# Kernel tuning notes

Measured on AMD Instinct MI355X. Metric: run time of the kernel, lower is better.

Reference implementation:

```python
import jax, jax.numpy as jnp
import numpy as np

B, LQ, LKV, E, H, D, P = 2, 2048, 2048, 1024, 16, 64, 64
NEG = -1e10


def setup_inputs() -> dict:
    key = jax.random.key(0)
    ks = jax.random.split(key, 8)
    inputs_q = jax.random.normal(ks[0], (B, LQ, E), jnp.float32)
    inputs_kv = jax.random.normal(ks[1], (B, LKV, E), jnp.float32)
    key_prefix = jax.random.normal(ks[2], (B, P, H, D), jnp.float32)
    value_prefix = jax.random.normal(ks[3], (B, P, H, D), jnp.float32)
    # causal mask, broadcastable over heads: [B, 1, LQ, LKV]
    mask = jnp.broadcast_to(jnp.tril(jnp.ones((LQ, LKV), bool)), (B, 1, LQ, LKV))
    scale = 1.0 / np.sqrt(E)  # fan_in variance scaling
    Wq = jax.random.normal(ks[4], (E, H, D), jnp.float32) * scale
    Wk = jax.random.normal(ks[5], (E, H, D), jnp.float32) * scale
    Wv = jax.random.normal(ks[6], (E, H, D), jnp.float32) * scale
    Wo = jax.random.normal(ks[7], (H, D, E), jnp.float32) * (1.0 / np.sqrt(H * D))
    return dict(inputs_q=inputs_q, inputs_kv=inputs_kv, key_prefix=key_prefix,
                value_prefix=value_prefix, mask=mask, Wq=Wq, Wk=Wk, Wv=Wv, Wo=Wo)


def reference(inputs_q, inputs_kv, key_prefix, value_prefix, mask, Wq, Wk, Wv, Wo):
    depth_scaling = jnp.sqrt(jnp.asarray(D, inputs_q.dtype))
    # query kernel is divided by sqrt(head_dim) at init -> fold into projection
    q = jnp.einsum('bqe,ehd->bqhd', inputs_q, Wq) / depth_scaling
    k = jnp.einsum('bke,ehd->bkhd', inputs_kv, Wk)
    v = jnp.einsum('bke,ehd->bkhd', inputs_kv, Wv)
    # prefix concat on the key/value length axis
    k = jnp.concatenate([key_prefix, k], axis=1)   # [B, P+LKV, H, D]
    v = jnp.concatenate([value_prefix, v], axis=1)
    # mask -> additive bias; prefix tokens get zero bias (always attendable)
    bias = jnp.where(mask, 0.0, NEG).astype(inputs_q.dtype)      # [B,1,LQ,LKV]
    prefix_bias = jnp.zeros(bias.shape[:-1] + (P,), bias.dtype)  # [B,1,LQ,P]
    bias = jnp.concatenate([prefix_bias, bias], axis=-1)         # [B,1,LQ,P+LKV]
    scores = jnp.einsum('bqhd,bkhd->bhqk', q, k) + bias
    probs = jax.nn.softmax(scores, axis=-1)
    ctx = jnp.einsum('bhqk,bkhd->bqhd', probs, v)
    return jnp.einsum('bqhd,hde->bqe', ctx, Wo)
```

## Files before the change

### kernel.cpp

```cpp
#include <hip/hip_runtime.h>
#include <hip/hip_bf16.h>

#define B_   2
#define LQ_  2048
#define LKV_ 2048
#define E_   1024
#define H_   16
#define D_   64
#define P_   64
#define LT_  (P_ + LKV_)
#define NEG_ -1e10f
#define LOG2E_ 1.4426950408889634f

typedef unsigned short ushort_t;
typedef unsigned int   uint_t;
typedef float f32x4   __attribute__((ext_vector_type(4)));
typedef float f32x16  __attribute__((ext_vector_type(16)));
typedef short bf16x8  __attribute__((ext_vector_type(8)));
typedef uint_t u32x4  __attribute__((ext_vector_type(4)));

__device__ __forceinline__ ushort_t f2bf(float f) {
    union { float f; uint_t u; } v; v.f = f;
    return (ushort_t)((v.u + 0x7fffu + ((v.u >> 16) & 1u)) >> 16);
}

__device__ __forceinline__ uint_t cvt_pk_bf16(float lo, float hi) {
    uint_t r;
    asm("v_cvt_pk_bf16_f32 %0, %1, %2" : "=v"(r) : "v"(lo), "v"(hi));
    return r;
}

__device__ __forceinline__ float exp2x(float x) {
    float r;
    asm("v_exp_f32 %0, %1" : "=v"(r) : "v"(x));
    return r;
}

__device__ __forceinline__ float bflo(uint_t u) {
    return __builtin_bit_cast(float, u << 16);
}
__device__ __forceinline__ float bfhi(uint_t u) {
    return __builtin_bit_cast(float, u & 0xFFFF0000u);
}


#define GLOAD16(gp, lp)                                                     \
    __builtin_amdgcn_global_load_lds(                                       \
        (const __attribute__((address_space(1))) void*)(gp),                \
        (__attribute__((address_space(3))) void*)(lp), 16, 0, 0)

__global__ __launch_bounds__(256) void prep(
    const float* __restrict__ iq, const float* __restrict__ ikv,
    const float* __restrict__ w0, const float* __restrict__ w1,
    const float* __restrict__ w2, const float* __restrict__ w3,
    const float* __restrict__ kp, const float* __restrict__ vp,
    ushort_t* __restrict__ Aq, ushort_t* __restrict__ Akv,
    ushort_t* __restrict__ d0, ushort_t* __restrict__ d1,
    ushort_t* __restrict__ d2, ushort_t* __restrict__ d3,
    ushort_t* __restrict__ kws, ushort_t* __restrict__ vws)
{
    __shared__ float t[32][33];
    const int blk = blockIdx.x;
    const int tid = threadIdx.x;

    if (blk < 8192) {
        const int idx = blk * 256 + tid;
        constexpr int HALF = 4096 * 1024 / 4;
        const float4 v = (idx < HALF) ? ((const float4*)iq)[idx]
                                      : ((const float4*)ikv)[idx - HALF];
        const uint2 p = make_uint2((uint_t)f2bf(v.x) | ((uint_t)f2bf(v.y) << 16),
                                   (uint_t)f2bf(v.z) | ((uint_t)f2bf(v.w) << 16));
        if (idx < HALF) ((uint2*)Aq)[idx] = p;
        else            ((uint2*)Akv)[idx - HALF] = p;
    } else if (blk < 12288) {
        const int tr = blk - 8192;
        const int bz = tr >> 10, rem = tr & 1023;
        const int x0 = (rem & 31) * 32, y0 = (rem >> 5) * 32;
        const float* S = (bz == 0) ? w0 : (bz == 1) ? w1 : (bz == 2) ? w2 : w3;
        ushort_t* D = (bz == 0) ? d0 : (bz == 1) ? d1 : (bz == 2) ? d2 : d3;
        const int tx = tid & 31, ty = tid >> 5;
        #pragma unroll
        for (int i = 0; i < 4; ++i)
            t[ty + i * 8][tx] = S[(size_t)(y0 + ty + i * 8) * 1024 + x0 + tx];
        __syncthreads();
        #pragma unroll
        for (int i = 0; i < 4; ++i)
            D[(size_t)(x0 + ty + i * 8) * 1024 + (y0 + tx)] =
                f2bf(t[tx][ty + i * 8]);
    } else {
        const int idx = (blk - 12288) * 256 + tid;
        const int d4 = idx & 15;
        const int h  = (idx >> 4) & 15;
        const int p  = (idx >> 8) & 63;
        const int b  = idx >> 14;
        const float4 kv = ((const float4*)kp)[idx];
        const float4 vv = ((const float4*)vp)[idx];
        const size_t kdst = ((size_t)(b * H_ + h) * LT_ + p) * D_ + d4 * 4;
        *(uint2*)(kws + kdst) =
            make_uint2((uint_t)f2bf(kv.x) | ((uint_t)f2bf(kv.y) << 16),
                       (uint_t)f2bf(kv.z) | ((uint_t)f2bf(kv.w) << 16));
        const float* vs = (const float*)&vv;
        #pragma unroll
        for (int i = 0; i < 4; ++i)
            vws[((size_t)(b * H_ + h) * D_ + d4 * 4 + i) * LT_ + p] = f2bf(vs[i]);
    }
}

__device__ __forceinline__ void gemm_core(const ushort_t* __restrict__ A,
                                          const ushort_t* __restrict__ Wt,
                                          ushort_t* As, ushort_t* Bs,
                                          int m0, int n0, f32x4 (*acc)[4])
{
    constexpr int K = 1024, NSTEP = 16;
    const int tid  = threadIdx.x;
    const int lane = tid & 63;
    const int wave = tid >> 6;
    const int l15 = lane & 15, lg = lane >> 4;
    const int wr = (wave >> 1) * 32;
    const int wc = (wave & 1) * 64;
    const uint_t xr = (uint_t)((l15 & 7) << 4);

    for (int i = 0; i < NSTEP; ++i) {
        const int k0 = i * 64;
        #pragma unroll
        for (int j = 0; j < 2; ++j) {
            const int c = j * 256 + tid;
            const int row = c >> 3, cc = c & 7;
            const size_t so = (size_t)row * K + k0 + ((cc ^ (row & 7)) * 8);
            GLOAD16(A + (size_t)m0 * K + so, (char*)As + (j * 256 + wave * 64) * 16);
        }
        #pragma unroll
        for (int j = 0; j < 4; ++j) {
            const int c = j * 256 + tid;
            const int row = c >> 3, cc = c & 7;
            const size_t so = (size_t)row * K + k0 + ((cc ^ (row & 7)) * 8);
            GLOAD16(Wt + (size_t)n0 * K + so, (char*)Bs + (j * 256 + wave * 64) * 16);
        }
        asm volatile("s_waitcnt vmcnt(0)" ::: "memory");
        __builtin_amdgcn_s_barrier();

        bf16x8 af[2][2], bfr[2][4];
        #pragma unroll
        for (int kt = 0; kt < 2; ++kt) {
            #pragma unroll
            for (int mt = 0; mt < 2; ++mt)
                af[kt][mt] = *(const bf16x8*)((const char*)As + (wr + mt * 16 + l15) * 128
                                              + ((kt * 64 + lg * 16) ^ xr));
            #pragma unroll
            for (int nt = 0; nt < 4; ++nt)
                bfr[kt][nt] = *(const bf16x8*)((const char*)Bs + (wc + nt * 16 + l15) * 128
                                               + ((kt * 64 + lg * 16) ^ xr));
        }
        #pragma unroll
        for (int mt = 0; mt < 2; ++mt)
            #pragma unroll
            for (int nt = 0; nt < 4; ++nt) {
                acc[mt][nt] = __builtin_amdgcn_mfma_f32_16x16x32_bf16(
                    af[0][mt], bfr[0][nt], acc[mt][nt], 0, 0, 0);
                acc[mt][nt] = __builtin_amdgcn_mfma_f32_16x16x32_bf16(
                    af[1][mt], bfr[1][nt], acc[mt][nt], 0, 0, 0);
            }

        __builtin_amdgcn_s_barrier();
    }
}

__global__ __launch_bounds__(256) void gemm_qkv(
    const ushort_t* __restrict__ Aq, const ushort_t* __restrict__ Akv,
    const ushort_t* __restrict__ WqT, const ushort_t* __restrict__ WkT,
    const ushort_t* __restrict__ WvT,
    ushort_t* __restrict__ qws, ushort_t* __restrict__ kws,
    ushort_t* __restrict__ vws)
{
    __shared__ __align__(16) ushort_t As[64 * 64];
    __shared__ __align__(16) ushort_t Bs[128 * 64];
    const int by = blockIdx.y, sel = by >> 3;
    const ushort_t* A  = sel ? Akv : Aq;
    const ushort_t* Wt = (sel == 0) ? WqT : (sel == 1) ? WkT : WvT;
    const float scale  = sel ? 1.0f : 0.125f * LOG2E_;
    const int m0 = blockIdx.x * 64, n0 = (by & 7) * 128;

    f32x4 acc[2][4];
    #pragma unroll
    for (int mt = 0; mt < 2; ++mt)
        #pragma unroll
        for (int nt = 0; nt < 4; ++nt) acc[mt][nt] = (f32x4)0.f;

    gemm_core(A, Wt, As, Bs, m0, n0, acc);

    const int lane = threadIdx.x & 63, wave = threadIdx.x >> 6;
    const int l15 = lane & 15, lg = lane >> 4;
    const int wr = (wave >> 1) * 32, wc = (wave & 1) * 64;

    if (sel == 2) {
        #pragma unroll
        for (int mt = 0; mt < 2; ++mt)
            #pragma unroll
            for (int nt = 0; nt < 4; ++nt) {
                const int n = n0 + wc + nt * 16 + l15;
                const int h = n >> 6, d = n & 63;
                const int m = m0 + wr + mt * 16 + lg * 4;
                const int bb = m >> 11, ll = m & 2047;
                const uint2 pk = make_uint2(
                    (uint_t)f2bf(acc[mt][nt][0]) | ((uint_t)f2bf(acc[mt][nt][1]) << 16),
                    (uint_t)f2bf(acc[mt][nt][2]) | ((uint_t)f2bf(acc[mt][nt][3]) << 16));
                *(uint2*)(vws + ((size_t)(bb * H_ + h) * D_ + d) * LT_ + P_ + ll) = pk;
            }
    } else {
        ushort_t* Cw     = (sel == 0) ? qws : kws;
        const int Lout   = (sel == 0) ? LQ_ : LT_;
        const int rowoff = (sel == 0) ? 0 : P_;
        #pragma unroll
        for (int mt = 0; mt < 2; ++mt)
            #pragma unroll
            for (int nt = 0; nt < 4; ++nt) {
                const int n = n0 + wc + nt * 16 + l15;
                const int h = n >> 6, d = n & 63;
                #pragma unroll
                for (int r = 0; r < 4; ++r) {
                    const int m = m0 + wr + mt * 16 + lg * 4 + r;
                    const int bb = m >> 11, ll = m & 2047;
                    Cw[(((size_t)(bb * H_ + h) * Lout) + (rowoff + ll)) * D_ + d] =
                        f2bf(acc[mt][nt][r] * scale);
                }
            }
    }
}

__global__ __launch_bounds__(256) void gemm_out(const ushort_t* __restrict__ A,
                                                const ushort_t* __restrict__ Wt,
                                                float* __restrict__ C)
{
    __shared__ __align__(16) ushort_t As[64 * 64];
    __shared__ __align__(16) ushort_t Bs[128 * 64];
    const int m0 = blockIdx.x * 64, n0 = blockIdx.y * 128;

    f32x4 acc[2][4];
    #pragma unroll
    for (int mt = 0; mt < 2; ++mt)
        #pragma unroll
        for (int nt = 0; nt < 4; ++nt) acc[mt][nt] = (f32x4)0.f;

    gemm_core(A, Wt, As, Bs, m0, n0, acc);

    const int lane = threadIdx.x & 63, wave = threadIdx.x >> 6;
    const int l15 = lane & 15, lg = lane >> 4;
    const int wr = (wave >> 1) * 32, wc = (wave & 1) * 64;
    #pragma unroll
    for (int mt = 0; mt < 2; ++mt)
        #pragma unroll
        for (int nt = 0; nt < 4; ++nt) {
            const int n = n0 + wc + nt * 16 + l15;
            #pragma unroll
            for (int r = 0; r < 4; ++r) {
                const int m = m0 + wr + mt * 16 + lg * 4 + r;
                C[(size_t)m * 1024 + n] = acc[mt][nt][r];
            }
        }
}

__global__ __launch_bounds__(256) void attn_mfma(const ushort_t* __restrict__ qws,
                                                 const ushort_t* __restrict__ kws,
                                                 const ushort_t* __restrict__ vws,
                                                 ushort_t* __restrict__ pO,
                                                 float* __restrict__ ml)
{
    const int tid  = threadIdx.x;
    const int lane = tid & 63;
    const int wave = tid >> 6;
    const int z    = blockIdx.x;
    const int slot = z >> 8;
    const int c    = z & 255;
    const int g    = c >> 5;
    const int bh   = c & 31;
    const int seg  = slot >> 1;
    const int qb   = (slot & 1) ? g : (15 - g);

    const ushort_t* Qg  = qws + (size_t)bh * LQ_ * D_;
    const ushort_t* Kg  = kws + (size_t)bh * LT_ * D_;
    const ushort_t* Vtg = vws + (size_t)bh * D_ * LT_;

    __shared__ __align__(16) ushort_t Ks[2 * 64 * 64];
    __shared__ __align__(16) ushort_t Vt[2 * 64 * 64];

    const int l31 = lane & 31;
    const int hi  = lane >> 5;
    const uint_t xsw = (uint_t)((l31 & 7) << 4);
    const int qbase = qb * 128 + wave * 32;
    const int q     = qbase + l31;
    const int qe    = qbase + 31;

    bf16x8 qf[4];
    #pragma unroll
    for (int kd = 0; kd < 4; ++kd)
        qf[kd] = *(const bf16x8*)(Qg + (size_t)q * D_ + kd * 16 + hi * 8);

    f32x16 acc[2];
    acc[0] = (f32x16)0.f;
    acc[1] = (f32x16)0.f;
    float lpreg = 0.f;

    const int ntile = 2 * qb + 3;
    const int i0    = seg ? (qb + 2) : 0;
    const int iend  = seg ? ntile : (qb + 2);

    auto STAGE = [&](int t, int par) {
        const int t0s = t * 64;
        char* kd = (char*)Ks + par * 8192;
        char* vd = (char*)Vt + par * 8192;
        #pragma unroll
        for (int i = 0; i < 2; ++i) {
            const int c2 = i * 256 + tid;
            const int rr = c2 >> 3, cc = c2 & 7;
            GLOAD16(Kg + (size_t)(t0s + rr) * D_ + ((cc ^ (rr & 7)) * 8),
                    kd + (i * 256 + wave * 64) * 16);
            GLOAD16(Vtg + (size_t)rr * LT_ + t0s + ((cc ^ (rr & 7)) * 8),
                    vd + (i * 256 + wave * 64) * 16);
        }
    };

    STAGE(i0, 0);
    STAGE(i0 + 1, 1);

    for (int i = i0; i < iend; ++i) {
        const int t0 = i * 64;
        const int cur = (i - i0) & 1;
        if (i + 1 < iend) {
            asm volatile("s_waitcnt vmcnt(4)" ::: "memory");
        } else {
            asm volatile("s_waitcnt vmcnt(0)" ::: "memory");
        }
        __builtin_amdgcn_s_barrier();

        if (t0 <= P_ + qe) {
            const char* KsB = (const char*)Ks + cur * 8192;
            const char* VtB = (const char*)Vt + cur * 8192;

            f32x16 sv[2];
            __builtin_amdgcn_s_setprio(1);
            #pragma unroll
            for (int th = 0; th < 2; ++th) {
                f32x16 zf = (f32x16)0.f;
                #pragma unroll
                for (int kd = 0; kd < 4; ++kd) {
                    const bf16x8 a = *(const bf16x8*)(
                        KsB + (th * 32 + l31) * 128 + ((kd * 32 + hi * 16) ^ xsw));
                    zf = __builtin_amdgcn_mfma_f32_32x32x16_bf16(a, qf[kd], zf, 0, 0, 0);
                }
                sv[th] = zf;
            }
            __builtin_amdgcn_s_setprio(0);

            if (t0 + 63 > P_ + qbase) {
                #pragma unroll
                for (int th = 0; th < 2; ++th)
                    #pragma unroll
                    for (int r = 0; r < 16; ++r) {
                        const int t = t0 + th * 32 + (r & 3) + 8 * (r >> 2) + 4 * hi;
                        if (!(t < P_ || (t - P_) <= q)) sv[th][r] += NEG_;
                    }
            }

            #pragma unroll
            for (int th = 0; th < 2; ++th)
                #pragma unroll
                for (int r = 0; r < 16; ++r)
                    sv[th][r] = exp2x(sv[th][r]);
            {
                float t16[16];
                #pragma unroll
                for (int r = 0; r < 16; ++r) t16[r] = sv[0][r] + sv[1][r];
                float t8[8];
                #pragma unroll
                for (int r = 0; r < 8; ++r) t8[r] = t16[r] + t16[r + 8];
                float t4[4];
                #pragma unroll
                for (int r = 0; r < 4; ++r) t4[r] = t8[r] + t8[r + 4];
                lpreg += (t4[0] + t4[1]) + (t4[2] + t4[3]);
            }

            bf16x8 pb[4];
            #pragma unroll
            for (int kt = 0; kt < 4; ++kt) {
                const int th = kt >> 1, base = (kt & 1) * 8;
                uint4 w;
                w.x = cvt_pk_bf16(sv[th][base + 0], sv[th][base + 1]);
                w.y = cvt_pk_bf16(sv[th][base + 2], sv[th][base + 3]);
                w.z = cvt_pk_bf16(sv[th][base + 4], sv[th][base + 5]);
                w.w = cvt_pk_bf16(sv[th][base + 6], sv[th][base + 7]);
                pb[kt] = __builtin_bit_cast(bf16x8, w);
            }

            __builtin_amdgcn_s_setprio(1);
            #pragma unroll
            for (int dh = 0; dh < 2; ++dh) {
                const char* rowp = VtB + (dh * 32 + l31) * 128 + 8 * hi;
                #pragma unroll
                for (int kt = 0; kt < 4; ++kt) {
                    const uint_t off = ((uint_t)(kt * 32)) ^ xsw;
                    const uint2 va = *(const uint2*)(rowp + off);
                    const uint2 vb = *(const uint2*)(rowp + (off ^ 16));
                    uint4 w;
                    w.x = va.x; w.y = va.y; w.z = vb.x; w.w = vb.y;
                    const bf16x8 vfr = __builtin_bit_cast(bf16x8, w);
                    acc[dh] = __builtin_amdgcn_mfma_f32_32x32x16_bf16(
                        vfr, pb[kt], acc[dh], 0, 0, 0);
                }
            }
            __builtin_amdgcn_s_setprio(0);
        }

        __builtin_amdgcn_s_barrier();
        if (i + 2 < iend) STAGE(i + 2, cur);
    }

    const float ltot = lpreg + __shfl_xor(lpreg, 32);
    const size_t qrow = (size_t)(seg * 32 + bh) * 2048 + q;
    #pragma unroll
    for (int dh = 0; dh < 2; ++dh)
        #pragma unroll
        for (int gg = 0; gg < 4; ++gg) {
            const int d = dh * 32 + gg * 8 + hi * 4;
            const uint2 pk = make_uint2(
                cvt_pk_bf16(acc[dh][4 * gg + 0], acc[dh][4 * gg + 1]),
                cvt_pk_bf16(acc[dh][4 * gg + 2], acc[dh][4 * gg + 3]));
            *(uint2*)(pO + qrow * 64 + d) = pk;
        }
    if (hi == 0)
        ml[qrow] = ltot;
}

__global__ __launch_bounds__(256) void attn_merge(const ushort_t* __restrict__ pO,
                                                  const float* __restrict__ ml,
                                                  ushort_t* __restrict__ ctx)
{
    const int idx = blockIdx.x * 256 + threadIdx.x;
    const int dg = idx & 15;
    const int q  = (idx >> 4) & 2047;
    const int bh = idx >> 15;
    const int b = bh >> 4, h = bh & 15;

    const size_t q0 = (size_t)bh * 2048 + q;
    const size_t q1 = (size_t)(32 + bh) * 2048 + q;
    const float inv = 1.0f / (ml[q0] + ml[q1]);

    const uint2 a0 = *(const uint2*)(pO + q0 * 64 + dg * 4);
    const uint2 a1 = *(const uint2*)(pO + q1 * 64 + dg * 4);
    const float o0 = (bflo(a0.x) + bflo(a1.x)) * inv;
    const float o1 = (bfhi(a0.x) + bfhi(a1.x)) * inv;
    const float o2 = (bflo(a0.y) + bflo(a1.y)) * inv;
    const float o3 = (bfhi(a0.y) + bfhi(a1.y)) * inv;

    const uint2 pk = make_uint2(
        (uint_t)f2bf(o0) | ((uint_t)f2bf(o1) << 16),
        (uint_t)f2bf(o2) | ((uint_t)f2bf(o3) << 16));
    *(uint2*)(ctx + (((size_t)b * LQ_ + q) * H_ + h) * D_ + dg * 4) = pk;
}

extern "C" void kernel_launch(void* const* d_in, const int* in_sizes, int n_in,
                              void* d_out, int out_size, void* d_ws, size_t ws_size,
                              hipStream_t stream)
{
    const float* inputs_q     = (const float*)d_in[0];
    const float* inputs_kv    = (const float*)d_in[1];
    const float* key_prefix   = (const float*)d_in[2];
    const float* value_prefix = (const float*)d_in[3];
    const float* Wq = (const float*)d_in[5];
    const float* Wk = (const float*)d_in[6];
    const float* Wv = (const float*)d_in[7];
    const float* Wo = (const float*)d_in[8];
    float* out = (float*)d_out;

    ushort_t* Aq  = (ushort_t*)d_ws;
    ushort_t* Akv = Aq  + (size_t)4096 * 1024;
    ushort_t* WqT = Akv + (size_t)4096 * 1024;
    ushort_t* WkT = WqT + (size_t)1024 * 1024;
    ushort_t* WvT = WkT + (size_t)1024 * 1024;
    ushort_t* WoT = WvT + (size_t)1024 * 1024;
    ushort_t* qws = WoT + (size_t)1024 * 1024;
    ushort_t* kws = qws + (size_t)B_ * H_ * LQ_ * D_;
    ushort_t* vws = kws + (size_t)B_ * H_ * LT_ * D_;
    ushort_t* ctx = vws + (size_t)B_ * H_ * LT_ * D_;

    ushort_t* pO    = Aq;
    float*    mlbuf = (float*)WqT;

    prep<<<12416, 256, 0, stream>>>(inputs_q, inputs_kv, Wq, Wk, Wv, Wo,
                                    key_prefix, value_prefix,
                                    Aq, Akv, WqT, WkT, WvT, WoT, kws, vws);
    gemm_qkv<<<dim3(64, 24), 256, 0, stream>>>(Aq, Akv, WqT, WkT, WvT,
                                               qws, kws, vws);
    attn_mfma<<<2 * B_ * H_ * (LQ_ / 128), 256, 0, stream>>>(qws, kws, vws,
                                                             pO, mlbuf);
    attn_merge<<<4096, 256, 0, stream>>>(pO, mlbuf, ctx);
    gemm_out<<<dim3(64, 8), 256, 0, stream>>>(ctx, WoT, out);
}
```

Measured before the change: 118.1 us.

## Split long causal query blocks into three KV segments for better load balance

The attention kernel now splits the heavier query blocks (qb 8-15) across three KV-range segments instead of two, so each workgroup does a smaller, more even share of the causal work. The grid grows from 1024 to 1280 blocks. Partial outputs of the third segment go to an extra buffer, and the merge kernel adds them in for those rows. This reduces tail imbalance on the long blocks, at the cost of more partial-result traffic and more re-reads of Q.

```diff
diff --git a/kernel.cpp b/kernel.cpp
--- a/kernel.cpp
+++ b/kernel.cpp
@@ -263,18 +263,32 @@
                                                  const ushort_t* __restrict__ kws,
                                                  const ushort_t* __restrict__ vws,
                                                  ushort_t* __restrict__ pO,
+                                                 ushort_t* __restrict__ pO2,
                                                  float* __restrict__ ml)
 {
     const int tid  = threadIdx.x;
     const int lane = tid & 63;
     const int wave = tid >> 6;
     const int z    = blockIdx.x;
-    const int slot = z >> 8;
-    const int c    = z & 255;
-    const int g    = c >> 5;
-    const int bh   = c & 31;
-    const int seg  = slot >> 1;
-    const int qb   = (slot & 1) ? g : (15 - g);
+
+    int qb, bh, s, i0, iend;
+    if (z < 768) {
+        s  = z >> 8;
+        qb = 8 + ((z >> 5) & 7);
+        bh = z & 31;
+        const int nt = 2 * qb + 3;
+        const int n0 = (nt + 2) / 3, n1 = (nt + 1) / 3;
+        i0   = (s == 0) ? 0 : ((s == 1) ? n0 : n0 + n1);
+        iend = (s == 0) ? n0 : ((s == 1) ? n0 + n1 : nt);
+    } else {
+        const int y = z - 768;
+        s  = y >> 8;
+        qb = 7 - ((y >> 5) & 7);
+        bh = y & 31;
+        const int nt = 2 * qb + 3;
+        i0   = s ? (qb + 2) : 0;
+        iend = s ? nt : (qb + 2);
+    }
 
     const ushort_t* Qg  = qws + (size_t)bh * LQ_ * D_;
     const ushort_t* Kg  = kws + (size_t)bh * LT_ * D_;
@@ -299,10 +313,6 @@
     acc[0] = (f32x16)0.f;
     acc[1] = (f32x16)0.f;
     float lpreg = 0.f;
-
-    const int ntile = 2 * qb + 3;
-    const int i0    = seg ? (qb + 2) : 0;
-    const int iend  = seg ? ntile : (qb + 2);
 
     auto STAGE = [&](int t, int par) {
         const int t0s = t * 64;
@@ -415,22 +425,39 @@
     }
 
     const float ltot = lpreg + __shfl_xor(lpreg, 32);
-    const size_t qrow = (size_t)(seg * 32 + bh) * 2048 + q;
-    #pragma unroll
-    for (int dh = 0; dh < 2; ++dh)
-        #pragma unroll
-        for (int gg = 0; gg < 4; ++gg) {
-            const int d = dh * 32 + gg * 8 + hi * 4;
-            const uint2 pk = make_uint2(
-                cvt_pk_bf16(acc[dh][4 * gg + 0], acc[dh][4 * gg + 1]),
-                cvt_pk_bf16(acc[dh][4 * gg + 2], acc[dh][4 * gg + 3]));
-            *(uint2*)(pO + qrow * 64 + d) = pk;
-        }
-    if (hi == 0)
-        ml[qrow] = ltot;
+    if (z < 768 && s == 2) {
+        const size_t e2 = (size_t)((qb - 8) * 32 + bh) * 128 + (q & 127);
+        #pragma unroll
+        for (int dh = 0; dh < 2; ++dh)
+            #pragma unroll
+            for (int gg = 0; gg < 4; ++gg) {
+                const int d = dh * 32 + gg * 8 + hi * 4;
+                const uint2 pk = make_uint2(
+                    cvt_pk_bf16(acc[dh][4 * gg + 0], acc[dh][4 * gg + 1]),
+                    cvt_pk_bf16(acc[dh][4 * gg + 2], acc[dh][4 * gg + 3]));
+                *(uint2*)(pO2 + e2 * 64 + d) = pk;
+            }
+        if (hi == 0)
+            ml[2 * 32 * 2048 + e2] = ltot;
+    } else {
+        const size_t qrow = (size_t)(s * 32 + bh) * 2048 + q;
+        #pragma unroll
+        for (int dh = 0; dh < 2; ++dh)
+            #pragma unroll
+            for (int gg = 0; gg < 4; ++gg) {
+                const int d = dh * 32 + gg * 8 + hi * 4;
+                const uint2 pk = make_uint2(
+                    cvt_pk_bf16(acc[dh][4 * gg + 0], acc[dh][4 * gg + 1]),
+                    cvt_pk_bf16(acc[dh][4 * gg + 2], acc[dh][4 * gg + 3]));
+                *(uint2*)(pO + qrow * 64 + d) = pk;
+            }
+        if (hi == 0)
+            ml[qrow] = ltot;
+    }
 }
 
 __global__ __launch_bounds__(256) void attn_merge(const ushort_t* __restrict__ pO,
+                                                  const ushort_t* __restrict__ pO2,
                                                   const float* __restrict__ ml,
                                                   ushort_t* __restrict__ ctx)
 {
@@ -439,21 +466,33 @@
     const int q  = (idx >> 4) & 2047;
     const int bh = idx >> 15;
     const int b = bh >> 4, h = bh & 15;
+    const int qb = q >> 7;
 
     const size_t q0 = (size_t)bh * 2048 + q;
     const size_t q1 = (size_t)(32 + bh) * 2048 + q;
-    const float inv = 1.0f / (ml[q0] + ml[q1]);
 
     const uint2 a0 = *(const uint2*)(pO + q0 * 64 + dg * 4);
     const uint2 a1 = *(const uint2*)(pO + q1 * 64 + dg * 4);
-    const float o0 = (bflo(a0.x) + bflo(a1.x)) * inv;
-    const float o1 = (bfhi(a0.x) + bfhi(a1.x)) * inv;
-    const float o2 = (bflo(a0.y) + bflo(a1.y)) * inv;
-    const float o3 = (bfhi(a0.y) + bfhi(a1.y)) * inv;
-
+    float l = ml[q0] + ml[q1];
+    float o0 = bflo(a0.x) + bflo(a1.x);
+    float o1 = bfhi(a0.x) + bfhi(a1.x);
+    float o2 = bflo(a0.y) + bflo(a1.y);
+    float o3 = bfhi(a0.y) + bfhi(a1.y);
+
+    if (qb >= 8) {
+        const size_t e2 = (size_t)((qb - 8) * 32 + bh) * 128 + (q & 127);
+        const uint2 a2 = *(const uint2*)(pO2 + e2 * 64 + dg * 4);
+        l  += ml[2 * 32 * 2048 + e2];
+        o0 += bflo(a2.x);
+        o1 += bfhi(a2.x);
+        o2 += bflo(a2.y);
+        o3 += bfhi(a2.y);
+    }
+
+    const float inv = 1.0f / l;
     const uint2 pk = make_uint2(
-        (uint_t)f2bf(o0) | ((uint_t)f2bf(o1) << 16),
-        (uint_t)f2bf(o2) | ((uint_t)f2bf(o3) << 16));
+        (uint_t)f2bf(o0 * inv) | ((uint_t)f2bf(o1 * inv) << 16),
+        (uint_t)f2bf(o2 * inv) | ((uint_t)f2bf(o3 * inv) << 16));
     *(uint2*)(ctx + (((size_t)b * LQ_ + q) * H_ + h) * D_ + dg * 4) = pk;
 }
 
@@ -483,15 +522,15 @@
     ushort_t* ctx = vws + (size_t)B_ * H_ * LT_ * D_;
 
     ushort_t* pO    = Aq;
-    float*    mlbuf = (float*)WqT;
+    ushort_t* pO2   = WqT;
+    float*    mlbuf = (float*)WvT;
 
     prep<<<12416, 256, 0, stream>>>(inputs_q, inputs_kv, Wq, Wk, Wv, Wo,
                                     key_prefix, value_prefix,
                                     Aq, Akv, WqT, WkT, WvT, WoT, kws, vws);
     gemm_qkv<<<dim3(64, 24), 256, 0, stream>>>(Aq, Akv, WqT, WkT, WvT,
                                                qws, kws, vws);
-    attn_mfma<<<2 * B_ * H_ * (LQ_ / 128), 256, 0, stream>>>(qws, kws, vws,
-                                                             pO, mlbuf);
-    attn_merge<<<4096, 256, 0, stream>>>(pO, mlbuf, ctx);
+    attn_mfma<<<1280, 256, 0, stream>>>(qws, kws, vws, pO, pO2, mlbuf);
+    attn_merge<<<4096, 256, 0, stream>>>(pO, pO2, mlbuf, ctx);
     gemm_out<<<dim3(64, 8), 256, 0, stream>>>(ctx, WoT, out);
 }
```

Result: slower. 120.5 us (+2.0%).
